# Kernel tuning notes

Measured on AMD Instinct MI355X. Metric: run time of the kernel, lower is better.

Reference implementation:

```python
import jax, jax.numpy as jnp
import numpy as np

N_E = 8192
E_DIM = 256
BETA = 0.25


def setup_inputs() -> dict:
    key = jax.random.key(0)
    k1, k2 = jax.random.split(key)
    z = jax.random.normal(k1, (8, 64, 64, E_DIM), dtype=jnp.float32)
    # embedding init: uniform(-1/n_e, 1/n_e) as in the torch module
    emb = jax.random.uniform(k2, (N_E, E_DIM), dtype=jnp.float32,
                             minval=-1.0 / N_E, maxval=1.0 / N_E)
    return {"z": z, "emb": emb}


def reference(z, emb):
    sg = jax.lax.stop_gradient
    zf = z.reshape(-1, E_DIM)  # [N, D]
    # squared euclidean distance (argmin-equivalent to torch.cdist)
    # d[n,k] = ||zf[n]||^2 - 2 zf[n].e[k] + ||e[k]||^2
    d = (jnp.sum(zf * zf, axis=1, keepdims=True)
         - 2.0 * (zf @ emb.T)
         + jnp.sum(emb * emb, axis=1))  # [N, n_e]
    idx = jnp.argmin(d, axis=1)  # [N]
    z_q = emb[idx].reshape(z.shape)
    loss_commit = BETA * jnp.mean((sg(z_q) - z) ** 2)
    loss_codebook = jnp.mean((z_q - sg(z)) ** 2)
    z_q_ste = z + sg(z_q - z)  # straight-through estimator
    return z_q_ste, loss_commit, loss_codebook, idx
```

## Files before the change

### kernel.cpp

```cpp
#include <hip/hip_runtime.h>


#define NROWS 32768
#define NE    8192
#define DDIM  256
#define BM    64
#define CAP   64
#define MARGIN 1e-4f
#define NCH   (NE / 64)

typedef __attribute__((ext_vector_type(8))) short bf16x8;
typedef __attribute__((ext_vector_type(4))) float f32x4;
typedef unsigned short u16;

__device__ __forceinline__ u16 f2bf(float f) {
  unsigned x = __float_as_uint(f);
  return (u16)((x + 0x7fffu + ((x >> 16) & 1u)) >> 16);
}

__device__ __forceinline__ void gload_lds16(const void* g, void* l) {
  __builtin_amdgcn_global_load_lds(
      (const __attribute__((address_space(1))) void*)g,
      (__attribute__((address_space(3))) void*)l, 16, 0, 0);
}

__global__ __launch_bounds__(256)
void vq_norms(const float* __restrict__ z, const float* __restrict__ emb,
              float* __restrict__ arow, float* __restrict__ cemb) {
  int gid  = blockIdx.x * 256 + threadIdx.x;
  int wid  = gid >> 6;
  int lane = threadIdx.x & 63;
  const float* src;
  float* dst;
  if (wid < NROWS) { src = z + (size_t)wid * DDIM;   dst = arow + wid; }
  else             { int r = wid - NROWS;
                     src = emb + (size_t)r * DDIM;   dst = cemb + r; }
  float4 v = *reinterpret_cast<const float4*>(src + lane * 4);
  float s = v.x * v.x + v.y * v.y;
  s += v.z * v.z;
  s += v.w * v.w;
  #pragma unroll
  for (int off = 1; off < 64; off <<= 1) s += __shfl_xor(s, off, 64);
  if (lane == 0) *dst = s;
}

__global__ __launch_bounds__(256)
void vq_cvt(const float* __restrict__ emb, u16* __restrict__ e16) {
  int o   = blockIdx.x * 256 + threadIdx.x;
  int g16 = o >> 9;
  int r   = o & 511;
  int s   = r >> 6;
  int l   = r & 63;
  int lg  = l >> 4, l15 = l & 15;
  int c   = g16 * 16 + l15;
  int kc  = s * 4 + lg;
  const float* src = emb + (size_t)c * DDIM + kc * 8;
  float4 v0 = *reinterpret_cast<const float4*>(src);
  float4 v1 = *reinterpret_cast<const float4*>(src + 4);
  u16 ov[8] = {f2bf(v0.x), f2bf(v0.y), f2bf(v0.z), f2bf(v0.w),
               f2bf(v1.x), f2bf(v1.y), f2bf(v1.z), f2bf(v1.w)};
  *reinterpret_cast<bf16x8*>(e16 + (size_t)o * 8) =
      *reinterpret_cast<bf16x8*>(ov);
}

__global__ __launch_bounds__(512, 4)
void vq_mfma(const float* __restrict__ z, const u16* __restrict__ e16,
             const float* __restrict__ arow, const float* __restrict__ cemb,
             unsigned* __restrict__ cnt, int* __restrict__ list) {
  __shared__ u16 Bs[2][64 * DDIM];

  const int t    = threadIdx.x;
  const int R0   = blockIdx.x * BM;
  const int lane = t & 63;
  const int wid  = t >> 6;
  const int wm   = wid >> 1;
  const int wn   = wid & 1;
  const int l15  = lane & 15;
  const int lg   = lane >> 4;

  bf16x8 af[8];
  const int row = R0 + wm * 16 + l15;
  {
    const float* zr = z + (size_t)row * DDIM;
    #pragma unroll
    for (int s = 0; s < 8; ++s) {
      const float* src = zr + (s * 4 + lg) * 8;
      float4 v0 = *reinterpret_cast<const float4*>(src);
      float4 v1 = *reinterpret_cast<const float4*>(src + 4);
      u16 o[8] = {f2bf(v0.x), f2bf(v0.y), f2bf(v0.z), f2bf(v0.w),
                  f2bf(v1.x), f2bf(v1.y), f2bf(v1.z), f2bf(v1.w)};
      af[s] = *reinterpret_cast<bf16x8*>(o);
    }
  }
  const float a_r = arow[row];
  float runmin = 3.4e38f;

  {
    const char* src = (const char*)e16;
    #pragma unroll
    for (int i = 0; i < 4; ++i) {
      int f = wid * 4 + i;
      gload_lds16(src + f * 1024 + lane * 16, (char*)&Bs[0][0] + f * 1024);
    }
  }
  __syncthreads();

  for (int ch = 0; ch < NCH; ++ch) {
    const int buf = ch & 1;
    const int C0  = ch * 64;

    if (ch + 1 < NCH) {
      const char* src = (const char*)e16 + (size_t)(ch + 1) * 32768;
      char* dst = (char*)&Bs[buf ^ 1][0];
      #pragma unroll
      for (int i = 0; i < 4; ++i) {
        int f = wid * 4 + i;
        gload_lds16(src + f * 1024 + lane * 16, dst + f * 1024);
      }
    }

    float4 cvv[2];
    #pragma unroll
    for (int ci = 0; ci < 2; ++ci)
      cvv[ci] = *reinterpret_cast<const float4*>(
          &cemb[C0 + wn * 32 + ci * 16 + lg * 4]);

    f32x4 acc[2];
    acc[0] = (f32x4){0.f, 0.f, 0.f, 0.f};
    acc[1] = (f32x4){0.f, 0.f, 0.f, 0.f};

    const u16* Bp = &Bs[buf][0];
    #pragma unroll
    for (int s = 0; s < 8; ++s) {
      bf16x8 bfr[2];
      #pragma unroll
      for (int ci = 0; ci < 2; ++ci)
        bfr[ci] = *reinterpret_cast<const bf16x8*>(
            &Bp[((wn * 2 + ci) * 8 + s) * 512 + lane * 8]);
      #pragma unroll
      for (int ci = 0; ci < 2; ++ci)
        acc[ci] = __builtin_amdgcn_mfma_f32_16x16x32_bf16(
            bfr[ci], af[s], acc[ci], 0, 0, 0);
    }

    __syncthreads();

    float lm = 3.4e38f;
    #pragma unroll
    for (int ci = 0; ci < 2; ++ci)
      #pragma unroll
      for (int r = 0; r < 4; ++r) {
        float dd = fmaf(-2.0f, acc[ci][r], a_r) + cvv[ci][r];
        lm = fminf(lm, dd);
      }
    float gm = fminf(lm, __shfl_xor(lm, 16, 64));
    gm = fminf(gm, __shfl_xor(gm, 32, 64));
    runmin = fminf(runmin, gm);
    float thr = runmin + MARGIN;
    if (lm <= thr) {
      const float h = 0.5f * (a_r - thr);
      #pragma unroll
      for (int ci = 0; ci < 2; ++ci)
        #pragma unroll
        for (int r = 0; r < 4; ++r)
          if (acc[ci][r] >= fmaf(0.5f, cvv[ci][r], h)) {
            int k = C0 + wn * 32 + ci * 16 + lg * 4 + r;
            unsigned p = atomicAdd(&cnt[row], 1u);
            if (p < CAP) list[(size_t)row * CAP + p] = k;
          }
    }
  }
}

__global__ __launch_bounds__(256)
void vq_rescore(const float* __restrict__ z, const float* __restrict__ emb,
                const float* __restrict__ arow, const float* __restrict__ cemb,
                const unsigned* __restrict__ cnt, const int* __restrict__ list,
                int* __restrict__ ws_idx) {
  const int row  = blockIdx.x * 4 + (threadIdx.x >> 6);
  const int lane = threadIdx.x & 63;
  const float a  = arow[row];
  const float4 zv = *reinterpret_cast<const float4*>(
      z + (size_t)row * DDIM + lane * 4);
  unsigned n = cnt[row];
  float bd = 3.4e38f;
  int   bk = 0;

  const bool fullscan = (n == 0 || n > CAP);
  const int  m = fullscan ? NE : (int)n;
  for (int i = 0; i < m; ++i) {
    int k = fullscan ? i : list[(size_t)row * CAP + i];
    const float4 ev = *reinterpret_cast<const float4*>(
        emb + (size_t)k * DDIM + lane * 4);
    float p = zv.x * ev.x;
    p = fmaf(zv.y, ev.y, p);
    p = fmaf(zv.z, ev.z, p);
    p = fmaf(zv.w, ev.w, p);
    #pragma unroll
    for (int off = 1; off < 64; off <<= 1) p += __shfl_xor(p, off, 64);
    float d = fmaf(-2.0f, p, a) + cemb[k];
    if (d < bd || (d == bd && k < bk)) { bd = d; bk = k; }
  }
  if (lane == 0) ws_idx[row] = bk;
}

__global__ __launch_bounds__(256)
void vq_gather(const float* __restrict__ z, const float* __restrict__ emb,
               const int* __restrict__ ws_idx,
               float* __restrict__ out_zq, float* __restrict__ out_idx,
               double* __restrict__ loss_accum) {
  __shared__ float part[4];
  const int t  = threadIdx.x;
  const int R0 = blockIdx.x * 64;
  float lsum = 0.0f;
  for (int rr = 0; rr < 64; ++rr) {
    const int kb = ws_idx[R0 + rr];
    const size_t gi = (size_t)(R0 + rr) * DDIM + t;
    const float zv = z[gi];
    const float qv = emb[(size_t)kb * DDIM + t];
    const float diff = qv - zv;
    out_zq[gi] = zv + diff;
    lsum = fmaf(diff, diff, lsum);
  }
  #pragma unroll
  for (int off = 1; off < 64; off <<= 1) lsum += __shfl_xor(lsum, off, 64);
  if ((t & 63) == 0) part[t >> 6] = lsum;
  __syncthreads();
  if (t == 0) {
    float tot = (part[0] + part[1]) + (part[2] + part[3]);
    atomicAdd(loss_accum, (double)tot);
  }
  if (t < 64) out_idx[R0 + t] = (float)ws_idx[R0 + t];
}

__global__ void vq_finalize(const double* __restrict__ loss_accum,
                            float* __restrict__ out_losses) {
  double m = *loss_accum / (double)((size_t)NROWS * DDIM);
  out_losses[0] = (float)(0.25 * m);
  out_losses[1] = (float)m;
}

extern "C" void kernel_launch(void* const* d_in, const int* in_sizes, int n_in,
                              void* d_out, int out_size, void* d_ws, size_t ws_size,
                              hipStream_t stream) {
  const float* z   = (const float*)d_in[0];
  const float* emb = (const float*)d_in[1];
  float* out        = (float*)d_out;
  float* out_zq     = out;
  float* out_losses = out + (size_t)NROWS * DDIM;
  float* out_idx    = out + (size_t)NROWS * DDIM + 2;

  double* loss_accum = (double*)d_ws;
  float*  arow   = (float*)((char*)d_ws + 256);
  float*  cemb   = arow + NROWS;
  int*    ws_idx = (int*)(cemb + NE);

  u16*      e16  = (u16*)d_out;
  int*      list = (int*)((char*)d_out + (4 << 20));
  unsigned* cnt  = (unsigned*)((char*)d_out + (12 << 20));

  hipMemsetAsync(d_ws, 0, 8, stream);
  hipMemsetAsync(cnt, 0, NROWS * sizeof(unsigned), stream);
  vq_norms<<<(NROWS + NE) / 4, 256, 0, stream>>>(z, emb, arow, cemb);
  vq_cvt<<<NE * 32 / 256, 256, 0, stream>>>(emb, e16);
  vq_mfma<<<NROWS / BM, 512, 0, stream>>>(z, e16, arow, cemb, cnt, list);
  vq_rescore<<<NROWS / 4, 256, 0, stream>>>(z, emb, arow, cemb, cnt, list, ws_idx);
  vq_gather<<<NROWS / 64, 256, 0, stream>>>(z, emb, ws_idx,
                                            out_zq, out_idx, loss_accum);
  vq_finalize<<<1, 1, 0, stream>>>(loss_accum, out_losses);
}
```

Before: 321.5 us.

## Switch distance GEMM to 32x32x16 MFMA with 128x128 block tiles

Doubles the row tile and codebook chunk to 128 and replaces 16x16x32 MFMA with 32x32x16 MFMA, so each wave computes a 32x64 tile. The bf16 codebook repacking kernel is re-laid out to match the new fragment layout. The aim is more reuse of each LDS-loaded fragment and fewer chunk iterations and barriers. In exchange the LDS footprint doubles to 128 KB per block, which together with the larger accumulators lowers occupancy, and the occupancy hint in launch bounds is dropped.

```diff
diff --git a/kernel.cpp b/kernel.cpp
--- a/kernel.cpp
+++ b/kernel.cpp
@@ -4,13 +4,13 @@
 #define NROWS 32768
 #define NE    8192
 #define DDIM  256
-#define BM    64
+#define BM    128
 #define CAP   64
 #define MARGIN 1e-4f
-#define NCH   (NE / 64)
-
-typedef __attribute__((ext_vector_type(8))) short bf16x8;
-typedef __attribute__((ext_vector_type(4))) float f32x4;
+#define NCH   (NE / 128)
+
+typedef __attribute__((ext_vector_type(8)))  short bf16x8;
+typedef __attribute__((ext_vector_type(16))) float f32x16;
 typedef unsigned short u16;
 
 __device__ __forceinline__ u16 f2bf(float f) {
@@ -46,15 +46,14 @@
 
 __global__ __launch_bounds__(256)
 void vq_cvt(const float* __restrict__ emb, u16* __restrict__ e16) {
-  int o   = blockIdx.x * 256 + threadIdx.x;
-  int g16 = o >> 9;
-  int r   = o & 511;
-  int s   = r >> 6;
-  int l   = r & 63;
-  int lg  = l >> 4, l15 = l & 15;
-  int c   = g16 * 16 + l15;
-  int kc  = s * 4 + lg;
-  const float* src = emb + (size_t)c * DDIM + kc * 8;
+  int o    = blockIdx.x * 256 + threadIdx.x;
+  int frag = o >> 6;
+  int l    = o & 63;
+  int g32  = frag >> 4;
+  int ks   = frag & 15;
+  int cand = g32 * 32 + (l & 31);
+  int k    = ks * 16 + (l >> 5) * 8;
+  const float* src = emb + (size_t)cand * DDIM + k;
   float4 v0 = *reinterpret_cast<const float4*>(src);
   float4 v1 = *reinterpret_cast<const float4*>(src + 4);
   u16 ov[8] = {f2bf(v0.x), f2bf(v0.y), f2bf(v0.z), f2bf(v0.w),
@@ -63,28 +62,28 @@
       *reinterpret_cast<bf16x8*>(ov);
 }
 
-__global__ __launch_bounds__(512, 4)
+__global__ __launch_bounds__(512)
 void vq_mfma(const float* __restrict__ z, const u16* __restrict__ e16,
              const float* __restrict__ arow, const float* __restrict__ cemb,
              unsigned* __restrict__ cnt, int* __restrict__ list) {
-  __shared__ u16 Bs[2][64 * DDIM];
+  __shared__ u16 Bs[2][128 * DDIM];
 
   const int t    = threadIdx.x;
   const int R0   = blockIdx.x * BM;
   const int lane = t & 63;
   const int wid  = t >> 6;
-  const int wm   = wid >> 1;
+  const int wg   = wid >> 1;
   const int wn   = wid & 1;
-  const int l15  = lane & 15;
-  const int lg   = lane >> 4;
-
-  bf16x8 af[8];
-  const int row = R0 + wm * 16 + l15;
+  const int l31  = lane & 31;
+  const int lh   = lane >> 5;
+
+  bf16x8 af[16];
+  const int row = R0 + wg * 32 + l31;
   {
     const float* zr = z + (size_t)row * DDIM;
     #pragma unroll
-    for (int s = 0; s < 8; ++s) {
-      const float* src = zr + (s * 4 + lg) * 8;
+    for (int s = 0; s < 16; ++s) {
+      const float* src = zr + s * 16 + lh * 8;
       float4 v0 = *reinterpret_cast<const float4*>(src);
       float4 v1 = *reinterpret_cast<const float4*>(src + 4);
       u16 o[8] = {f2bf(v0.x), f2bf(v0.y), f2bf(v0.z), f2bf(v0.w),
@@ -98,8 +97,8 @@
   {
     const char* src = (const char*)e16;
     #pragma unroll
-    for (int i = 0; i < 4; ++i) {
-      int f = wid * 4 + i;
+    for (int i = 0; i < 8; ++i) {
+      int f = wid * 8 + i;
       gload_lds16(src + f * 1024 + lane * 16, (char*)&Bs[0][0] + f * 1024);
     }
   }
@@ -107,39 +106,43 @@
 
   for (int ch = 0; ch < NCH; ++ch) {
     const int buf = ch & 1;
-    const int C0  = ch * 64;
+    const int C0  = ch * 128;
 
     if (ch + 1 < NCH) {
-      const char* src = (const char*)e16 + (size_t)(ch + 1) * 32768;
+      const char* src = (const char*)e16 + (size_t)(ch + 1) * 65536;
       char* dst = (char*)&Bs[buf ^ 1][0];
       #pragma unroll
-      for (int i = 0; i < 4; ++i) {
-        int f = wid * 4 + i;
+      for (int i = 0; i < 8; ++i) {
+        int f = wid * 8 + i;
         gload_lds16(src + f * 1024 + lane * 16, dst + f * 1024);
       }
     }
 
-    float4 cvv[2];
+    float4 cvv[2][4];
     #pragma unroll
     for (int ci = 0; ci < 2; ++ci)
-      cvv[ci] = *reinterpret_cast<const float4*>(
-          &cemb[C0 + wn * 32 + ci * 16 + lg * 4]);
-
-    f32x4 acc[2];
-    acc[0] = (f32x4){0.f, 0.f, 0.f, 0.f};
-    acc[1] = (f32x4){0.f, 0.f, 0.f, 0.f};
+      #pragma unroll
+      for (int q = 0; q < 4; ++q)
+        cvv[ci][q] = *reinterpret_cast<const float4*>(
+            &cemb[C0 + wn * 64 + ci * 32 + q * 8 + lh * 4]);
+
+    f32x16 acc[2];
+    #pragma unroll
+    for (int ci = 0; ci < 2; ++ci)
+      #pragma unroll
+      for (int r = 0; r < 16; ++r) acc[ci][r] = 0.0f;
 
     const u16* Bp = &Bs[buf][0];
     #pragma unroll
-    for (int s = 0; s < 8; ++s) {
+    for (int s = 0; s < 16; ++s) {
       bf16x8 bfr[2];
       #pragma unroll
       for (int ci = 0; ci < 2; ++ci)
         bfr[ci] = *reinterpret_cast<const bf16x8*>(
-            &Bp[((wn * 2 + ci) * 8 + s) * 512 + lane * 8]);
+            &Bp[(((wn * 2 + ci) * 16) + s) * 512 + lane * 8]);
       #pragma unroll
       for (int ci = 0; ci < 2; ++ci)
-        acc[ci] = __builtin_amdgcn_mfma_f32_16x16x32_bf16(
+        acc[ci] = __builtin_amdgcn_mfma_f32_32x32x16_bf16(
             bfr[ci], af[s], acc[ci], 0, 0, 0);
     }
 
@@ -149,12 +152,11 @@
     #pragma unroll
     for (int ci = 0; ci < 2; ++ci)
       #pragma unroll
-      for (int r = 0; r < 4; ++r) {
-        float dd = fmaf(-2.0f, acc[ci][r], a_r) + cvv[ci][r];
+      for (int r = 0; r < 16; ++r) {
+        float dd = fmaf(-2.0f, acc[ci][r], a_r) + cvv[ci][r >> 2][r & 3];
         lm = fminf(lm, dd);
       }
-    float gm = fminf(lm, __shfl_xor(lm, 16, 64));
-    gm = fminf(gm, __shfl_xor(gm, 32, 64));
+    float gm = fminf(lm, __shfl_xor(lm, 32, 64));
     runmin = fminf(runmin, gm);
     float thr = runmin + MARGIN;
     if (lm <= thr) {
@@ -162,9 +164,9 @@
       #pragma unroll
       for (int ci = 0; ci < 2; ++ci)
         #pragma unroll
-        for (int r = 0; r < 4; ++r)
-          if (acc[ci][r] >= fmaf(0.5f, cvv[ci][r], h)) {
-            int k = C0 + wn * 32 + ci * 16 + lg * 4 + r;
+        for (int r = 0; r < 16; ++r)
+          if (acc[ci][r] >= fmaf(0.5f, cvv[ci][r >> 2][r & 3], h)) {
+            int k = C0 + wn * 64 + ci * 32 + (r & 3) + 8 * (r >> 2) + 4 * lh;
             unsigned p = atomicAdd(&cnt[row], 1u);
             if (p < CAP) list[(size_t)row * CAP + p] = k;
           }
```

New measurement: 332.5 us. 3.4% more time.

## Switch distance screening GEMM from bf16 to scaled fp8 MFMA

Applied to the files above, without the earlier changes.

Converts z and the codebook to fp8 (codebook scaled up by a fixed factor) and uses the fp8 16x16x32 MFMA for the candidate screening pass, halving codebook bytes in LDS and global traffic. The distance and threshold formulas are rescaled to match, and the margin and per-row candidate cap are enlarged to absorb the larger fp8 error. Exact rescoring still picks the final index, but more candidates per row can be emitted, which adds atomics and rescoring work, and a fixed scale tied to the embedding init range risks missing true minima if values fall outside it.

```diff
diff --git a/kernel.cpp b/kernel.cpp
--- a/kernel.cpp
+++ b/kernel.cpp
@@ -5,17 +5,23 @@
 #define NE    8192
 #define DDIM  256
 #define BM    64
-#define CAP   64
-#define MARGIN 1e-4f
+#define CAP   128
+#define MARGIN 1e-3f
 #define NCH   (NE / 64)
-
-typedef __attribute__((ext_vector_type(8))) short bf16x8;
+#define ESCALE 8192.0f
+#define DSCALE (1.0f/4096.0f)
+#define USCALE 4096.0f
+
 typedef __attribute__((ext_vector_type(4))) float f32x4;
-typedef unsigned short u16;
-
-__device__ __forceinline__ u16 f2bf(float f) {
-  unsigned x = __float_as_uint(f);
-  return (u16)((x + 0x7fffu + ((x >> 16) & 1u)) >> 16);
+typedef unsigned long long u64;
+
+__device__ __forceinline__ u64 pack_fp8x8(float4 v0, float4 v1, float s) {
+  int w0 = 0, w1 = 0;
+  w0 = __builtin_amdgcn_cvt_pk_fp8_f32(v0.x * s, v0.y * s, w0, false);
+  w0 = __builtin_amdgcn_cvt_pk_fp8_f32(v0.z * s, v0.w * s, w0, true);
+  w1 = __builtin_amdgcn_cvt_pk_fp8_f32(v1.x * s, v1.y * s, w1, false);
+  w1 = __builtin_amdgcn_cvt_pk_fp8_f32(v1.z * s, v1.w * s, w1, true);
+  return ((u64)(unsigned)w1 << 32) | (unsigned)w0;
 }
 
 __device__ __forceinline__ void gload_lds16(const void* g, void* l) {
@@ -45,29 +51,25 @@
 }
 
 __global__ __launch_bounds__(256)
-void vq_cvt(const float* __restrict__ emb, u16* __restrict__ e16) {
-  int o   = blockIdx.x * 256 + threadIdx.x;
-  int g16 = o >> 9;
-  int r   = o & 511;
-  int s   = r >> 6;
-  int l   = r & 63;
-  int lg  = l >> 4, l15 = l & 15;
-  int c   = g16 * 16 + l15;
-  int kc  = s * 4 + lg;
-  const float* src = emb + (size_t)c * DDIM + kc * 8;
+void vq_cvt8(const float* __restrict__ emb, u64* __restrict__ e8) {
+  int o    = blockIdx.x * 256 + threadIdx.x;
+  int frag = o >> 6;
+  int l    = o & 63;
+  int g16  = frag >> 3;
+  int s    = frag & 7;
+  int cand = g16 * 16 + (l & 15);
+  int k    = s * 32 + (l >> 4) * 8;
+  const float* src = emb + (size_t)cand * DDIM + k;
   float4 v0 = *reinterpret_cast<const float4*>(src);
   float4 v1 = *reinterpret_cast<const float4*>(src + 4);
-  u16 ov[8] = {f2bf(v0.x), f2bf(v0.y), f2bf(v0.z), f2bf(v0.w),
-               f2bf(v1.x), f2bf(v1.y), f2bf(v1.z), f2bf(v1.w)};
-  *reinterpret_cast<bf16x8*>(e16 + (size_t)o * 8) =
-      *reinterpret_cast<bf16x8*>(ov);
+  e8[o] = pack_fp8x8(v0, v1, ESCALE);
 }
 
 __global__ __launch_bounds__(512, 4)
-void vq_mfma(const float* __restrict__ z, const u16* __restrict__ e16,
+void vq_mfma(const float* __restrict__ z, const u64* __restrict__ e8,
              const float* __restrict__ arow, const float* __restrict__ cemb,
              unsigned* __restrict__ cnt, int* __restrict__ list) {
-  __shared__ u16 Bs[2][64 * DDIM];
+  __shared__ char Bs[2][16384];
 
   const int t    = threadIdx.x;
   const int R0   = blockIdx.x * BM;
@@ -78,29 +80,27 @@
   const int l15  = lane & 15;
   const int lg   = lane >> 4;
 
-  bf16x8 af[8];
+  u64 af[8];
   const int row = R0 + wm * 16 + l15;
   {
     const float* zr = z + (size_t)row * DDIM;
     #pragma unroll
     for (int s = 0; s < 8; ++s) {
-      const float* src = zr + (s * 4 + lg) * 8;
+      const float* src = zr + s * 32 + lg * 8;
       float4 v0 = *reinterpret_cast<const float4*>(src);
       float4 v1 = *reinterpret_cast<const float4*>(src + 4);
-      u16 o[8] = {f2bf(v0.x), f2bf(v0.y), f2bf(v0.z), f2bf(v0.w),
-                  f2bf(v1.x), f2bf(v1.y), f2bf(v1.z), f2bf(v1.w)};
-      af[s] = *reinterpret_cast<bf16x8*>(o);
+      af[s] = pack_fp8x8(v0, v1, 1.0f);
     }
   }
   const float a_r = arow[row];
   float runmin = 3.4e38f;
 
   {
-    const char* src = (const char*)e16;
-    #pragma unroll
-    for (int i = 0; i < 4; ++i) {
-      int f = wid * 4 + i;
-      gload_lds16(src + f * 1024 + lane * 16, (char*)&Bs[0][0] + f * 1024);
+    const char* src = (const char*)e8;
+    #pragma unroll
+    for (int i = 0; i < 2; ++i) {
+      int f = wid * 2 + i;
+      gload_lds16(src + f * 1024 + lane * 16, &Bs[0][0] + f * 1024);
     }
   }
   __syncthreads();
@@ -110,11 +110,11 @@
     const int C0  = ch * 64;
 
     if (ch + 1 < NCH) {
-      const char* src = (const char*)e16 + (size_t)(ch + 1) * 32768;
-      char* dst = (char*)&Bs[buf ^ 1][0];
-      #pragma unroll
-      for (int i = 0; i < 4; ++i) {
-        int f = wid * 4 + i;
+      const char* src = (const char*)e8 + (size_t)(ch + 1) * 16384;
+      char* dst = &Bs[buf ^ 1][0];
+      #pragma unroll
+      for (int i = 0; i < 2; ++i) {
+        int f = wid * 2 + i;
         gload_lds16(src + f * 1024 + lane * 16, dst + f * 1024);
       }
     }
@@ -129,18 +129,18 @@
     acc[0] = (f32x4){0.f, 0.f, 0.f, 0.f};
     acc[1] = (f32x4){0.f, 0.f, 0.f, 0.f};
 
-    const u16* Bp = &Bs[buf][0];
+    const char* Bp = &Bs[buf][0];
     #pragma unroll
     for (int s = 0; s < 8; ++s) {
-      bf16x8 bfr[2];
+      u64 bfr[2];
       #pragma unroll
       for (int ci = 0; ci < 2; ++ci)
-        bfr[ci] = *reinterpret_cast<const bf16x8*>(
-            &Bp[((wn * 2 + ci) * 8 + s) * 512 + lane * 8]);
+        bfr[ci] = *reinterpret_cast<const u64*>(
+            Bp + (((wn * 2 + ci) * 8 + s) * 512) + lane * 8);
       #pragma unroll
       for (int ci = 0; ci < 2; ++ci)
-        acc[ci] = __builtin_amdgcn_mfma_f32_16x16x32_bf16(
-            bfr[ci], af[s], acc[ci], 0, 0, 0);
+        acc[ci] = __builtin_amdgcn_mfma_f32_16x16x32_fp8_fp8(
+            (long)bfr[ci], (long)af[s], acc[ci], 0, 0, 0);
     }
 
     __syncthreads();
@@ -150,7 +150,7 @@
     for (int ci = 0; ci < 2; ++ci)
       #pragma unroll
       for (int r = 0; r < 4; ++r) {
-        float dd = fmaf(-2.0f, acc[ci][r], a_r) + cvv[ci][r];
+        float dd = fmaf(-DSCALE, acc[ci][r], a_r) + cvv[ci][r];
         lm = fminf(lm, dd);
       }
     float gm = fminf(lm, __shfl_xor(lm, 16, 64));
@@ -158,12 +158,12 @@
     runmin = fminf(runmin, gm);
     float thr = runmin + MARGIN;
     if (lm <= thr) {
-      const float h = 0.5f * (a_r - thr);
+      const float h = USCALE * (a_r - thr);
       #pragma unroll
       for (int ci = 0; ci < 2; ++ci)
         #pragma unroll
         for (int r = 0; r < 4; ++r)
-          if (acc[ci][r] >= fmaf(0.5f, cvv[ci][r], h)) {
+          if (acc[ci][r] >= fmaf(USCALE, cvv[ci][r], h)) {
             int k = C0 + wn * 32 + ci * 16 + lg * 4 + r;
             unsigned p = atomicAdd(&cnt[row], 1u);
             if (p < CAP) list[(size_t)row * CAP + p] = k;
@@ -255,15 +255,15 @@
   float*  cemb   = arow + NROWS;
   int*    ws_idx = (int*)(cemb + NE);
 
-  u16*      e16  = (u16*)d_out;
-  int*      list = (int*)((char*)d_out + (4 << 20));
-  unsigned* cnt  = (unsigned*)((char*)d_out + (12 << 20));
+  u64*      e8   = (u64*)d_out;
+  int*      list = (int*)((char*)d_out + (2 << 20));
+  unsigned* cnt  = (unsigned*)((char*)d_out + (18 << 20));
 
   hipMemsetAsync(d_ws, 0, 8, stream);
   hipMemsetAsync(cnt, 0, NROWS * sizeof(unsigned), stream);
   vq_norms<<<(NROWS + NE) / 4, 256, 0, stream>>>(z, emb, arow, cemb);
-  vq_cvt<<<NE * 32 / 256, 256, 0, stream>>>(emb, e16);
-  vq_mfma<<<NROWS / BM, 512, 0, stream>>>(z, e16, arow, cemb, cnt, list);
+  vq_cvt8<<<NE * 32 / 256, 256, 0, stream>>>(emb, e8);
+  vq_mfma<<<NROWS / BM, 512, 0, stream>>>(z, e8, arow, cemb, cnt, list);
   vq_rescore<<<NROWS / 4, 256, 0, stream>>>(z, emb, arow, cemb, cnt, list, ws_idx);
   vq_gather<<<NROWS / 64, 256, 0, stream>>>(z, emb, ws_idx,
                                             out_zq, out_idx, loss_accum);
```

Measured after the change: 481.4 us. +49.7%, slower.

## Triple-buffer codebook chunks with vmcnt waits and vectorize gather kernel

Applied to the files above, without the earlier changes.

The MFMA distance kernel now streams 32-code chunks through a three-slot LDS ring, keeping two chunks in flight. It waits with explicit s_waitcnt vmcnt plus one raw barrier per chunk, replacing the two __syncthreads of the double-buffered 64-code scheme. Each wave now issues one MFMA per k-step instead of two, which halves LDS use and may allow more occupancy or overlap, at the cost of more loop iterations and barriers. Separately, the gather kernel uses float4 loads and stores with one wave per row instead of scalar per-thread accesses.

```diff
diff --git a/kernel.cpp b/kernel.cpp
--- a/kernel.cpp
+++ b/kernel.cpp
@@ -7,7 +7,7 @@
 #define BM    64
 #define CAP   64
 #define MARGIN 1e-4f
-#define NCH   (NE / 64)
+#define NCH   (NE / 32)
 
 typedef __attribute__((ext_vector_type(8))) short bf16x8;
 typedef __attribute__((ext_vector_type(4))) float f32x4;
@@ -67,7 +67,7 @@
 void vq_mfma(const float* __restrict__ z, const u16* __restrict__ e16,
              const float* __restrict__ arow, const float* __restrict__ cemb,
              unsigned* __restrict__ cnt, int* __restrict__ list) {
-  __shared__ u16 Bs[2][64 * DDIM];
+  __shared__ char Bs[3][16384];
 
   const int t    = threadIdx.x;
   const int R0   = blockIdx.x * BM;
@@ -98,61 +98,55 @@
   {
     const char* src = (const char*)e16;
     #pragma unroll
-    for (int i = 0; i < 4; ++i) {
-      int f = wid * 4 + i;
-      gload_lds16(src + f * 1024 + lane * 16, (char*)&Bs[0][0] + f * 1024);
-    }
-  }
-  __syncthreads();
+    for (int i = 0; i < 2; ++i) {
+      int f = wid * 2 + i;
+      gload_lds16(src + f * 1024 + lane * 16, &Bs[0][0] + f * 1024);
+    }
+    #pragma unroll
+    for (int i = 0; i < 2; ++i) {
+      int f = wid * 2 + i;
+      gload_lds16(src + 16384 + f * 1024 + lane * 16, &Bs[1][0] + f * 1024);
+    }
+  }
 
   for (int ch = 0; ch < NCH; ++ch) {
-    const int buf = ch & 1;
-    const int C0  = ch * 64;
-
-    if (ch + 1 < NCH) {
-      const char* src = (const char*)e16 + (size_t)(ch + 1) * 32768;
-      char* dst = (char*)&Bs[buf ^ 1][0];
+    if (ch == NCH - 1) {
+      asm volatile("s_waitcnt vmcnt(0)" ::: "memory");
+    } else {
+      asm volatile("s_waitcnt vmcnt(2)" ::: "memory");
+    }
+    __builtin_amdgcn_s_barrier();
+    asm volatile("" ::: "memory");
+
+    if (ch + 2 < NCH) {
+      const char* src = (const char*)e16 + (size_t)(ch + 2) * 16384;
+      char* dst = &Bs[(ch + 2) % 3][0];
       #pragma unroll
-      for (int i = 0; i < 4; ++i) {
-        int f = wid * 4 + i;
+      for (int i = 0; i < 2; ++i) {
+        int f = wid * 2 + i;
         gload_lds16(src + f * 1024 + lane * 16, dst + f * 1024);
       }
     }
 
-    float4 cvv[2];
-    #pragma unroll
-    for (int ci = 0; ci < 2; ++ci)
-      cvv[ci] = *reinterpret_cast<const float4*>(
-          &cemb[C0 + wn * 32 + ci * 16 + lg * 4]);
-
-    f32x4 acc[2];
-    acc[0] = (f32x4){0.f, 0.f, 0.f, 0.f};
-    acc[1] = (f32x4){0.f, 0.f, 0.f, 0.f};
-
-    const u16* Bp = &Bs[buf][0];
+    const int C0 = ch * 32;
+    const float4 cvv = *reinterpret_cast<const float4*>(
+        &cemb[C0 + wn * 16 + lg * 4]);
+
+    f32x4 acc = (f32x4){0.f, 0.f, 0.f, 0.f};
+    const char* Bp = &Bs[ch % 3][0];
     #pragma unroll
     for (int s = 0; s < 8; ++s) {
-      bf16x8 bfr[2];
-      #pragma unroll
-      for (int ci = 0; ci < 2; ++ci)
-        bfr[ci] = *reinterpret_cast<const bf16x8*>(
-            &Bp[((wn * 2 + ci) * 8 + s) * 512 + lane * 8]);
-      #pragma unroll
-      for (int ci = 0; ci < 2; ++ci)
-        acc[ci] = __builtin_amdgcn_mfma_f32_16x16x32_bf16(
-            bfr[ci], af[s], acc[ci], 0, 0, 0);
-    }
-
-    __syncthreads();
+      const bf16x8 bfr = *reinterpret_cast<const bf16x8*>(
+          Bp + (wn * 8 + s) * 1024 + lane * 16);
+      acc = __builtin_amdgcn_mfma_f32_16x16x32_bf16(bfr, af[s], acc, 0, 0, 0);
+    }
 
     float lm = 3.4e38f;
     #pragma unroll
-    for (int ci = 0; ci < 2; ++ci)
-      #pragma unroll
-      for (int r = 0; r < 4; ++r) {
-        float dd = fmaf(-2.0f, acc[ci][r], a_r) + cvv[ci][r];
-        lm = fminf(lm, dd);
-      }
+    for (int r = 0; r < 4; ++r) {
+      float dd = fmaf(-2.0f, acc[r], a_r) + cvv[r];
+      lm = fminf(lm, dd);
+    }
     float gm = fminf(lm, __shfl_xor(lm, 16, 64));
     gm = fminf(gm, __shfl_xor(gm, 32, 64));
     runmin = fminf(runmin, gm);
@@ -160,14 +154,12 @@
     if (lm <= thr) {
       const float h = 0.5f * (a_r - thr);
       #pragma unroll
-      for (int ci = 0; ci < 2; ++ci)
-        #pragma unroll
-        for (int r = 0; r < 4; ++r)
-          if (acc[ci][r] >= fmaf(0.5f, cvv[ci][r], h)) {
-            int k = C0 + wn * 32 + ci * 16 + lg * 4 + r;
-            unsigned p = atomicAdd(&cnt[row], 1u);
-            if (p < CAP) list[(size_t)row * CAP + p] = k;
-          }
+      for (int r = 0; r < 4; ++r)
+        if (acc[r] >= fmaf(0.5f, cvv[r], h)) {
+          int k = C0 + wn * 16 + lg * 4 + r;
+          unsigned p = atomicAdd(&cnt[row], 1u);
+          if (p < CAP) list[(size_t)row * CAP + p] = k;
+        }
     }
   }
 }
@@ -210,21 +202,32 @@
                float* __restrict__ out_zq, float* __restrict__ out_idx,
                double* __restrict__ loss_accum) {
   __shared__ float part[4];
-  const int t  = threadIdx.x;
-  const int R0 = blockIdx.x * 64;
+  const int t    = threadIdx.x;
+  const int wid  = t >> 6;
+  const int lane = t & 63;
+  const int R0   = blockIdx.x * 64;
   float lsum = 0.0f;
-  for (int rr = 0; rr < 64; ++rr) {
-    const int kb = ws_idx[R0 + rr];
-    const size_t gi = (size_t)(R0 + rr) * DDIM + t;
-    const float zv = z[gi];
-    const float qv = emb[(size_t)kb * DDIM + t];
-    const float diff = qv - zv;
-    out_zq[gi] = zv + diff;
-    lsum = fmaf(diff, diff, lsum);
+  for (int rr = 0; rr < 16; ++rr) {
+    const int row = R0 + rr * 4 + wid;
+    const int kb  = ws_idx[row];
+    const float4 zv = *reinterpret_cast<const float4*>(
+        z + (size_t)row * DDIM + lane * 4);
+    const float4 ev = *reinterpret_cast<const float4*>(
+        emb + (size_t)kb * DDIM + lane * 4);
+    float dx = ev.x - zv.x;
+    float dy = ev.y - zv.y;
+    float dz = ev.z - zv.z;
+    float dw = ev.w - zv.w;
+    float4 o = {zv.x + dx, zv.y + dy, zv.z + dz, zv.w + dw};
+    *reinterpret_cast<float4*>(out_zq + (size_t)row * DDIM + lane * 4) = o;
+    lsum = fmaf(dx, dx, lsum);
+    lsum = fmaf(dy, dy, lsum);
+    lsum = fmaf(dz, dz, lsum);
+    lsum = fmaf(dw, dw, lsum);
   }
   #pragma unroll
   for (int off = 1; off < 64; off <<= 1) lsum += __shfl_xor(lsum, off, 64);
-  if ((t & 63) == 0) part[t >> 6] = lsum;
+  if (lane == 0) part[wid] = lsum;
   __syncthreads();
   if (t == 0) {
     float tot = (part[0] + part[1]) + (part[2] + part[3]);
```

New measurement: 376.6 us. 1.17x slower.
